# Kernel tuning notes

Hardware: AMD Instinct MI355X
Metric: run time of the kernel (lower is better)

Reference implementation:

```python
import jax, jax.numpy as jnp
import numpy as np

N = 8192
IN_F = 512
OUT_F = 64
ALPHA = 0.2  # LeakyReLU negative slope
NEG_INF = -9e15


def setup_inputs() -> dict:
    key = jax.random.key(0)
    k1, k2, k3, k4 = jax.random.split(key, 4)
    x = jax.random.normal(k1, (N, IN_F), dtype=jnp.float32)
    adj = jax.random.randint(k2, (N, N), 0, 2, dtype=jnp.int32)
    # xavier_uniform with gain=1.414
    def xavier(k, shape, gain=1.414):
        fan_in, fan_out = shape[0], shape[1]
        a = gain * np.sqrt(6.0 / (fan_in + fan_out))
        return jax.random.uniform(k, shape, jnp.float32, -a, a)
    W = xavier(k3, (IN_F, OUT_F))
    a = xavier(k4, (2 * OUT_F, 1))
    return {"x": x, "adj": adj, "W": W, "a": a}


def reference(x, adj, W, a):
    h = x @ W  # [N, F]
    f = W.shape[1]
    # e[i,j] = leakyrelu([h_i, h_j] @ a) = leakyrelu(h_i@a1 + h_j@a2)
    e1 = h @ a[:f, 0]   # [N]
    e2 = h @ a[f:, 0]   # [N]
    e = jax.nn.leaky_relu(e1[:, None] + e2[None, :], negative_slope=ALPHA)  # [N, N]
    scores = jnp.where(adj > 0, e, NEG_INF)
    attention = jax.nn.softmax(scores, axis=1)  # dropout p=0.0 -> identity
    h_prime = attention @ h  # [N, F]
    return jax.nn.elu(h_prime)  # concat=True
```

## Files before the change

kernel.cpp:

```cpp
#include <hip/hip_runtime.h>
#include <hip/hip_bf16.h>

#define NN 8192
#define KF 512
#define FF 64
#define GAT_ALPHA 0.2f
#define MSHIFT 20.0f
#define LOG2E 1.44269504f

#define JCH 512
#define NCH (NN / JCH)
#define PST 520

#define EXP2F(x) __builtin_amdgcn_exp2f(x)

typedef __attribute__((ext_vector_type(8))) __bf16 bf16x8;
typedef __attribute__((ext_vector_type(4))) float f32x4;

__global__ __launch_bounds__(256) void gat_linear(
    const float* __restrict__ x, const float* __restrict__ W,
    const float* __restrict__ av, __hip_bfloat16* __restrict__ ht,
    float* __restrict__ e1, float* __restrict__ e2)
{
    __shared__ float xs[32][33];
    __shared__ float Ws[32][64];
    __shared__ float ep[2][32][17];

    const int t  = threadIdx.x;
    const int fq = t & 15;
    const int rq = t >> 4;
    const int i0 = blockIdx.x * 32;

    const int kl = t & 31, r0 = t >> 5;
    const int fw = t & 63, kq = t >> 6;

    float acc[2][4] = {};

    for (int kt = 0; kt < KF; kt += 32) {
        #pragma unroll
        for (int m = 0; m < 4; ++m)
            xs[kl][r0 + 8 * m] = x[(size_t)(i0 + r0 + 8 * m) * KF + kt + kl];
        #pragma unroll
        for (int m = 0; m < 8; ++m)
            Ws[kq + 4 * m][fw] = W[(size_t)(kt + kq + 4 * m) * FF + fw];
        __syncthreads();
        #pragma unroll
        for (int kk = 0; kk < 32; ++kk) {
            float x0 = xs[kk][rq * 2];
            float x1 = xs[kk][rq * 2 + 1];
            f32x4 wv = *(const f32x4*)&Ws[kk][fq * 4];
            #pragma unroll
            for (int v = 0; v < 4; ++v) {
                acc[0][v] += x0 * wv[v];
                acc[1][v] += x1 * wv[v];
            }
        }
        __syncthreads();
    }

    #pragma unroll
    for (int v = 0; v < 4; ++v) {
        int f = fq * 4 + v;
        union { ushort2 q; __hip_bfloat16 h[2]; } pk;
        pk.h[0] = __float2bfloat16(acc[0][v]);
        pk.h[1] = __float2bfloat16(acc[1][v]);
        *(ushort2*)&ht[(size_t)f * NN + i0 + rq * 2] = pk.q;
    }

    f32x4 a1v = *(const f32x4*)&av[fq * 4];
    f32x4 a2v = *(const f32x4*)&av[64 + fq * 4];
    #pragma unroll
    for (int u = 0; u < 2; ++u) {
        float s1 = 0.f, s2 = 0.f;
        #pragma unroll
        for (int v = 0; v < 4; ++v) {
            s1 += acc[u][v] * a1v[v];
            s2 += acc[u][v] * a2v[v];
        }
        ep[0][rq * 2 + u][fq] = s1;
        ep[1][rq * 2 + u][fq] = s2;
    }
    __syncthreads();
    if (t < 32) {
        float s1 = 0.f, s2 = 0.f;
        #pragma unroll
        for (int q = 0; q < 16; ++q) { s1 += ep[0][t][q]; s2 += ep[1][t][q]; }
        e1[i0 + t] = s1 * LOG2E;
        e2[i0 + t] = s2 * LOG2E;
    }
}

__global__ __launch_bounds__(256, 2) void gat_attn(
    const int* __restrict__ adj, const __hip_bfloat16* __restrict__ ht,
    const float* __restrict__ e1, const float* __restrict__ e2,
    float* __restrict__ out)
{
    __shared__ __hip_bfloat16 ps[2][16][PST];
    __shared__ float l_red[16];

    const int t    = threadIdx.x;
    const int ii   = t >> 4;
    const int jq   = t & 15;
    const int i0   = blockIdx.x * 16;
    const int lane = t & 63;
    const int wv   = t >> 6;
    const int n16  = lane & 15;
    const int quad = lane >> 4;

    const float e1L = e1[i0 + ii];
    float ms = e1L + MSHIFT * LOG2E;
    const float miL = ms > 0.f ? ms : GAT_ALPHA * ms;

    if (t < 16) l_red[t] = 0.f;

    const int*   arow = adj + (size_t)(i0 + ii) * NN + jq * 4;
    const float* e2p  = e2 + jq * 4;
    const __hip_bfloat16* hbase = ht + (size_t)(wv * 16 + n16) * NN + quad * 8;

    int4 aj[8];
    #pragma unroll
    for (int g = 0; g < 8; ++g)
        aj[g] = *(const int4*)(arow + g * 64);

    float lpart = 0.f;
    f32x4 dacc = {0.f, 0.f, 0.f, 0.f};

    for (int c = 0; c < NCH; ++c) {
        const int buf = c & 1;
        #pragma unroll
        for (int g = 0; g < 8; ++g) {
            float4 e_ = *(const float4*)(e2p + c * JCH + g * 64);
            int4   a_ = aj[g];
            union { uint2 u; __hip_bfloat16 h[4]; } pk;
            float s_, p_;
            s_ = e1L + e_.x; s_ = s_ > 0.f ? s_ : GAT_ALPHA * s_;
            p_ = a_.x > 0 ? EXP2F(s_ - miL) : 0.f;
            pk.h[0] = __float2bfloat16(p_); lpart += __bfloat162float(pk.h[0]);
            s_ = e1L + e_.y; s_ = s_ > 0.f ? s_ : GAT_ALPHA * s_;
            p_ = a_.y > 0 ? EXP2F(s_ - miL) : 0.f;
            pk.h[1] = __float2bfloat16(p_); lpart += __bfloat162float(pk.h[1]);
            s_ = e1L + e_.z; s_ = s_ > 0.f ? s_ : GAT_ALPHA * s_;
            p_ = a_.z > 0 ? EXP2F(s_ - miL) : 0.f;
            pk.h[2] = __float2bfloat16(p_); lpart += __bfloat162float(pk.h[2]);
            s_ = e1L + e_.w; s_ = s_ > 0.f ? s_ : GAT_ALPHA * s_;
            p_ = a_.w > 0 ? EXP2F(s_ - miL) : 0.f;
            pk.h[3] = __float2bfloat16(p_); lpart += __bfloat162float(pk.h[3]);
            *(uint2*)&ps[buf][ii][g * 64 + jq * 4] = pk.u;
        }
        if (c + 1 < NCH) {
            #pragma unroll
            for (int g = 0; g < 8; ++g)
                aj[g] = *(const int4*)(arow + (c + 1) * JCH + g * 64);
        }
        __syncthreads();
        const __hip_bfloat16* hb = hbase + (size_t)c * JCH;
        #pragma unroll
        for (int kk = 0; kk < JCH / 32; ++kk) {
            bf16x8 af = *(const bf16x8*)&ps[buf][n16][kk * 32 + quad * 8];
            bf16x8 bf = *(const bf16x8*)(hb + kk * 32);
            dacc = __builtin_amdgcn_mfma_f32_16x16x32_bf16(af, bf, dacc, 0, 0, 0);
        }
    }

    atomicAdd(&l_red[ii], lpart);
    __syncthreads();

    #pragma unroll
    for (int r = 0; r < 4; ++r) {
        int row = quad * 4 + r;
        float hv = dacc[r] / l_red[row];
        float o = hv > 0.f ? hv : __expf(hv) - 1.f;
        out[(size_t)(i0 + row) * FF + wv * 16 + n16] = o;
    }
}

extern "C" void kernel_launch(void* const* d_in, const int* in_sizes, int n_in,
                              void* d_out, int out_size, void* d_ws, size_t ws_size,
                              hipStream_t stream) {
    const float* x   = (const float*)d_in[0];
    const int*   adj = (const int*)d_in[1];
    const float* W   = (const float*)d_in[2];
    const float* av  = (const float*)d_in[3];
    float* out = (float*)d_out;

    char* wsb = (char*)d_ws;
    __hip_bfloat16* ht = (__hip_bfloat16*)wsb;
    float* e1 = (float*)(wsb + (1 << 20));
    float* e2 = e1 + NN;

    gat_linear<<<256, 256, 0, stream>>>(x, W, av, ht, e1, e2);
    gat_attn<<<512, 256, 0, stream>>>(adj, ht, e1, e2, out);
}
```

Measured before the change: 478.6 us.

## Split attention columns across blocks with atomic partial accumulation and epilogue

Splits the j dimension of the attention kernel four ways so each row-tile is handled by four blocks, raising the grid from 512 to 2048 blocks. Partial numerators and row sums are combined with global float atomics into a zeroed workspace, and a new epilogue kernel applies normalization and ELU. It also drops the double-buffered shared tile for a single buffer with an extra barrier and raises the occupancy hint. The aim is better latency hiding for the adj-bandwidth-bound stream, at the cost of two extra launches, atomic traffic and a non-deterministic summation order.

New measurement: 430.0 us. 1.11x faster.

```diff
diff --git a/kernel.cpp b/kernel.cpp
--- a/kernel.cpp
+++ b/kernel.cpp
@@ -8,14 +8,19 @@
 #define MSHIFT 20.0f
 #define LOG2E 1.44269504f
 
+#define JSPLIT 4
 #define JCH 512
-#define NCH (NN / JCH)
+#define NCHB (NN / JSPLIT / JCH)
 #define PST 520
 
 #define EXP2F(x) __builtin_amdgcn_exp2f(x)
 
 typedef __attribute__((ext_vector_type(8))) __bf16 bf16x8;
 typedef __attribute__((ext_vector_type(4))) float f32x4;
+
+__global__ __launch_bounds__(256) void zero_ws(float4* __restrict__ p) {
+    p[blockIdx.x * 256 + threadIdx.x] = make_float4(0.f, 0.f, 0.f, 0.f);
+}
 
 __global__ __launch_bounds__(256) void gat_linear(
     const float* __restrict__ x, const float* __restrict__ W,
@@ -90,22 +95,23 @@
     }
 }
 
-__global__ __launch_bounds__(256, 2) void gat_attn(
+__global__ __launch_bounds__(256, 8) void gat_attn(
     const int* __restrict__ adj, const __hip_bfloat16* __restrict__ ht,
     const float* __restrict__ e1, const float* __restrict__ e2,
-    float* __restrict__ out)
+    float* __restrict__ acc, float* __restrict__ lsum)
 {
-    __shared__ __hip_bfloat16 ps[2][16][PST];
+    __shared__ __hip_bfloat16 ps[16][PST];
     __shared__ float l_red[16];
 
-    const int t    = threadIdx.x;
-    const int ii   = t >> 4;
-    const int jq   = t & 15;
-    const int i0   = blockIdx.x * 16;
-    const int lane = t & 63;
-    const int wv   = t >> 6;
-    const int n16  = lane & 15;
-    const int quad = lane >> 4;
+    const int t     = threadIdx.x;
+    const int ii    = t >> 4;
+    const int jq    = t & 15;
+    const int i0    = (blockIdx.x >> 2) * 16;
+    const int jbase = (blockIdx.x & 3) * (NN / JSPLIT);
+    const int lane  = t & 63;
+    const int wv    = t >> 6;
+    const int n16   = lane & 15;
+    const int quad  = lane >> 4;
 
     const float e1L = e1[i0 + ii];
     float ms = e1L + MSHIFT * LOG2E;
@@ -113,9 +119,9 @@
 
     if (t < 16) l_red[t] = 0.f;
 
-    const int*   arow = adj + (size_t)(i0 + ii) * NN + jq * 4;
-    const float* e2p  = e2 + jq * 4;
-    const __hip_bfloat16* hbase = ht + (size_t)(wv * 16 + n16) * NN + quad * 8;
+    const int*   arow = adj + (size_t)(i0 + ii) * NN + jbase + jq * 4;
+    const float* e2p  = e2 + jbase + jq * 4;
+    const __hip_bfloat16* hbase = ht + (size_t)(wv * 16 + n16) * NN + jbase + quad * 8;
 
     int4 aj[8];
     #pragma unroll
@@ -125,8 +131,7 @@
     float lpart = 0.f;
     f32x4 dacc = {0.f, 0.f, 0.f, 0.f};
 
-    for (int c = 0; c < NCH; ++c) {
-        const int buf = c & 1;
+    for (int c = 0; c < NCHB; ++c) {
         #pragma unroll
         for (int g = 0; g < 8; ++g) {
             float4 e_ = *(const float4*)(e2p + c * JCH + g * 64);
@@ -145,9 +150,9 @@
             s_ = e1L + e_.w; s_ = s_ > 0.f ? s_ : GAT_ALPHA * s_;
             p_ = a_.w > 0 ? EXP2F(s_ - miL) : 0.f;
             pk.h[3] = __float2bfloat16(p_); lpart += __bfloat162float(pk.h[3]);
-            *(uint2*)&ps[buf][ii][g * 64 + jq * 4] = pk.u;
-        }
-        if (c + 1 < NCH) {
+            *(uint2*)&ps[ii][g * 64 + jq * 4] = pk.u;
+        }
+        if (c + 1 < NCHB) {
             #pragma unroll
             for (int g = 0; g < 8; ++g)
                 aj[g] = *(const int4*)(arow + (c + 1) * JCH + g * 64);
@@ -156,22 +161,38 @@
         const __hip_bfloat16* hb = hbase + (size_t)c * JCH;
         #pragma unroll
         for (int kk = 0; kk < JCH / 32; ++kk) {
-            bf16x8 af = *(const bf16x8*)&ps[buf][n16][kk * 32 + quad * 8];
+            bf16x8 af = *(const bf16x8*)&ps[n16][kk * 32 + quad * 8];
             bf16x8 bf = *(const bf16x8*)(hb + kk * 32);
             dacc = __builtin_amdgcn_mfma_f32_16x16x32_bf16(af, bf, dacc, 0, 0, 0);
         }
+        __syncthreads();
     }
 
     atomicAdd(&l_red[ii], lpart);
     __syncthreads();
+    if (t < 16) atomicAdd(&lsum[i0 + t], l_red[t]);
 
     #pragma unroll
     for (int r = 0; r < 4; ++r) {
         int row = quad * 4 + r;
-        float hv = dacc[r] / l_red[row];
-        float o = hv > 0.f ? hv : __expf(hv) - 1.f;
-        out[(size_t)(i0 + row) * FF + wv * 16 + n16] = o;
-    }
+        atomicAdd(&acc[(size_t)(i0 + row) * FF + wv * 16 + n16], dacc[r]);
+    }
+}
+
+__global__ __launch_bounds__(256) void gat_epilogue(
+    const float* __restrict__ acc, const float* __restrict__ lsum,
+    float* __restrict__ out)
+{
+    int idx = (blockIdx.x * 256 + threadIdx.x) * 4;
+    float li = 1.f / lsum[idx >> 6];
+    f32x4 a = *(const f32x4*)(acc + idx);
+    f32x4 o;
+    #pragma unroll
+    for (int v = 0; v < 4; ++v) {
+        float hv = a[v] * li;
+        o[v] = hv > 0.f ? hv : __expf(hv) - 1.f;
+    }
+    *(f32x4*)(out + idx) = o;
 }
 
 extern "C" void kernel_launch(void* const* d_in, const int* in_sizes, int n_in,
@@ -185,9 +206,13 @@
 
     char* wsb = (char*)d_ws;
     __hip_bfloat16* ht = (__hip_bfloat16*)wsb;
-    float* e1 = (float*)(wsb + (1 << 20));
-    float* e2 = e1 + NN;
-
+    float* e1  = (float*)(wsb + (1 << 20));
+    float* e2  = e1 + NN;
+    float* acc = e2 + NN;
+    float* lsum = acc + (size_t)NN * FF;
+
+    zero_ws<<<(NN * FF + NN) / 1024, 256, 0, stream>>>((float4*)acc);
     gat_linear<<<256, 256, 0, stream>>>(x, W, av, ht, e1, e2);
-    gat_attn<<<512, 256, 0, stream>>>(adj, ht, e1, e2, out);
-}
+    gat_attn<<<NN / 16 * JSPLIT, 256, 0, stream>>>(adj, ht, e1, e2, acc, lsum);
+    gat_epilogue<<<NN * FF / 1024, 256, 0, stream>>>(acc, lsum, out);
+}
```
